# Kernel optimization log

Measured on AMD Instinct MI355X. Metric: run time of the kernel, lower is better.

The kernel has to match this reference:

```python
import jax, jax.numpy as jnp
import numpy as np

D_MODEL = 2048
N_HEADS = 16
QK_ROPE = 64
QK_NOPE = 128
KV_LORA = 512
V_DIM = 128
QK_DIM = QK_ROPE + QK_NOPE
RMS_EPS = 1.1920928955078125e-07  # torch fp32 finfo.eps (nn.RMSNorm default eps=None)


def apply_rope(x, base=10000.0):
    # x: [B, S, H, D] ; torchtune-style interleaved-pair rotary
    B, S, H, D = x.shape
    freqs = 1.0 / (base ** (jnp.arange(0, D, 2, dtype=jnp.float32) / D))  # [D/2]
    t = jnp.arange(S, dtype=jnp.float32)[:, None] * freqs[None, :]        # [S, D/2]
    cos = jnp.cos(t)[None, :, None, :]
    sin = jnp.sin(t)[None, :, None, :]
    x1 = x[..., 0::2]
    x2 = x[..., 1::2]
    out = jnp.stack([x1 * cos - x2 * sin, x2 * cos + x1 * sin], axis=-1)
    return out.reshape(B, S, H, D).astype(x.dtype)


def setup_inputs() -> dict:
    key = jax.random.key(0)
    ks = jax.random.split(key, 6)
    s = lambda fan_in: 1.0 / np.sqrt(fan_in)
    x = jax.random.normal(ks[0], (2, 2048, D_MODEL), dtype=jnp.float32)
    Wq = jax.random.normal(ks[1], (D_MODEL, N_HEADS * QK_DIM), dtype=jnp.float32) * s(D_MODEL)
    Wkv_a = jax.random.normal(ks[2], (D_MODEL, KV_LORA + QK_ROPE), dtype=jnp.float32) * s(D_MODEL)
    kv_norm_w = jnp.ones((KV_LORA,), dtype=jnp.float32)
    Wkv_b = jax.random.normal(ks[3], (KV_LORA, N_HEADS * (QK_NOPE + V_DIM)), dtype=jnp.float32) * s(KV_LORA)
    Wo = jax.random.normal(ks[4], (N_HEADS * V_DIM, D_MODEL), dtype=jnp.float32) * s(N_HEADS * V_DIM)
    return {"x": x, "Wq": Wq, "Wkv_a": Wkv_a, "kv_norm_w": kv_norm_w, "Wkv_b": Wkv_b, "Wo": Wo}


def reference(x, Wq, Wkv_a, kv_norm_w, Wkv_b, Wo):
    B, S, _ = x.shape
    # queries: split nope/rope, rotary on rope slice only
    q = (x @ Wq).reshape(B, S, N_HEADS, QK_DIM)
    q_nope, q_rope = q[..., :QK_NOPE], q[..., QK_NOPE:]
    q = jnp.concatenate([q_nope, apply_rope(q_rope)], axis=-1)  # [B,S,H,QK_DIM]
    # compressed kv + decoupled rope key
    kv = x @ Wkv_a                                              # [B,S,KV_LORA+QK_ROPE]
    c_kv, k_rope = kv[..., :KV_LORA], kv[..., KV_LORA:]
    k_rope = apply_rope(k_rope.reshape(B, S, 1, QK_ROPE))       # [B,S,1,QK_ROPE]
    # RMSNorm on compressed latent, then decompress
    c_kv = c_kv * jax.lax.rsqrt(jnp.mean(c_kv * c_kv, axis=-1, keepdims=True) + RMS_EPS) * kv_norm_w
    kv = (c_kv @ Wkv_b).reshape(B, S, N_HEADS, QK_NOPE + V_DIM)
    k_nope, v = kv[..., :QK_NOPE], kv[..., QK_NOPE:]
    k = jnp.concatenate([k_nope, jnp.broadcast_to(k_rope, (B, S, N_HEADS, QK_ROPE))], axis=-1)
    # causal SDPA over sequence dim
    scale = 1.0 / np.sqrt(QK_DIM)
    scores = jnp.einsum('bqhd,bkhd->bhqk', q, k) * scale        # [B,H,S,S]
    mask = jnp.tril(jnp.ones((S, S), dtype=bool))
    scores = jnp.where(mask, scores, jnp.finfo(scores.dtype).min)
    attn = jax.nn.softmax(scores, axis=-1)
    out = jnp.einsum('bhqk,bkhd->bqhd', attn, v).reshape(B, S, N_HEADS * V_DIM)
    return out @ Wo
```

## Files before the change

kernel.cpp:

```cpp
#include <hip/hip_runtime.h>
#include <hip/hip_bf16.h>
#include <math.h>

#define BATCH   2
#define SEQ     2048
#define DM      2048
#define NH      16
#define QKR     64
#define QKN     128
#define KVL     512
#define VD      128
#define QKD     192
#define KVA_LD  640
#define RMS_EPS 1.1920928955078125e-07f

typedef __bf16 bf16x8 __attribute__((ext_vector_type(8)));
typedef float  f32x4  __attribute__((ext_vector_type(4)));

__device__ __forceinline__ void async16(const __bf16* g, __bf16* l)
{
    __builtin_amdgcn_global_load_lds(
        (__attribute__((address_space(1))) unsigned int*)g,
        (__attribute__((address_space(3))) unsigned int*)l,
        16, 0, 0);
}

__global__ __launch_bounds__(256) void f32_to_bf16(const float* __restrict__ src,
                                                   __bf16* __restrict__ dst)
{
    int i = (blockIdx.x * 256 + threadIdx.x) * 4;
    float4 v = *reinterpret_cast<const float4*>(src + i);
    dst[i + 0] = (__bf16)v.x;
    dst[i + 1] = (__bf16)v.y;
    dst[i + 2] = (__bf16)v.z;
    dst[i + 3] = (__bf16)v.w;
}

__global__ __launch_bounds__(256) void transpose_w(const float* __restrict__ W,
                                                   __bf16* __restrict__ Wt,
                                                   int K, int N)
{
    __shared__ float t[64][65];
    const int n0 = blockIdx.x * 64, k0 = blockIdx.y * 64;
    const int tid = threadIdx.x;
    #pragma unroll
    for (int i = 0; i < 16; ++i) {
        int flat = i * 256 + tid;
        int kl = flat >> 6, nl = flat & 63;
        t[kl][nl] = (n0 + nl < N) ? W[(size_t)(k0 + kl) * N + n0 + nl] : 0.f;
    }
    __syncthreads();
    #pragma unroll
    for (int i = 0; i < 16; ++i) {
        int flat = i * 256 + tid;
        int nl = flat >> 6, kl = flat & 63;
        Wt[(size_t)(n0 + nl) * K + k0 + kl] = (__bf16)t[kl][nl];
    }
}

template<typename OT>
__global__ __launch_bounds__(256) void gemm_bf16(const __bf16* __restrict__ A,
                                                 const __bf16* __restrict__ Bt,
                                                 OT* __restrict__ C,
                                                 int K, int lda, int ldb, int ldc)
{
    __shared__ __bf16 As[128 * 32];
    __shared__ __bf16 Bs[128 * 32];
    const int tid = threadIdx.x;
    const int lane = tid & 63, wave = tid >> 6;
    const int n = lane & 15, quad = lane >> 4;
    const int row0 = blockIdx.y * 128, col0 = blockIdx.x * 128;
    const int wm = (wave >> 1) * 64, wn = (wave & 1) * 64;

    f32x4 acc[4][4];
    #pragma unroll
    for (int mi = 0; mi < 4; ++mi)
        #pragma unroll
        for (int ni = 0; ni < 4; ++ni)
            #pragma unroll
            for (int r = 0; r < 4; ++r) acc[mi][ni][r] = 0.f;

    const __bf16* Ag0 = A  + (size_t)(row0 + (tid >> 2)) * lda + (tid & 3) * 8;
    const __bf16* Bg0 = Bt + (size_t)(col0 + (tid >> 2)) * ldb + (tid & 3) * 8;
    const __bf16* Ag1 = Ag0 + (size_t)64 * lda;
    const __bf16* Bg1 = Bg0 + (size_t)64 * ldb;
    __bf16* As0 = As + tid * 8;        __bf16* As1 = As + (tid + 256) * 8;
    __bf16* Bs0 = Bs + tid * 8;        __bf16* Bs1 = Bs + (tid + 256) * 8;

    for (int k0 = 0; k0 < K; k0 += 32) {
        __syncthreads();
        async16(Ag0 + k0, As0);
        async16(Ag1 + k0, As1);
        async16(Bg0 + k0, Bs0);
        async16(Bg1 + k0, Bs1);
        __syncthreads();

        bf16x8 af[4], bfr[4];
        #pragma unroll
        for (int mi = 0; mi < 4; ++mi)
            af[mi] = *reinterpret_cast<const bf16x8*>(&As[(wm + mi * 16 + n) * 32 + quad * 8]);
        #pragma unroll
        for (int ni = 0; ni < 4; ++ni)
            bfr[ni] = *reinterpret_cast<const bf16x8*>(&Bs[(wn + ni * 16 + n) * 32 + quad * 8]);
        #pragma unroll
        for (int mi = 0; mi < 4; ++mi)
            #pragma unroll
            for (int ni = 0; ni < 4; ++ni)
                acc[mi][ni] = __builtin_amdgcn_mfma_f32_16x16x32_bf16(af[mi], bfr[ni], acc[mi][ni], 0, 0, 0);
    }

    #pragma unroll
    for (int mi = 0; mi < 4; ++mi)
        #pragma unroll
        for (int r = 0; r < 4; ++r) {
            OT* cp = C + (size_t)(row0 + wm + mi * 16 + quad * 4 + r) * ldc + col0 + wn + n;
            #pragma unroll
            for (int ni = 0; ni < 4; ++ni)
                cp[ni * 16] = (OT)acc[mi][ni][r];
        }
}

__global__ __launch_bounds__(256) void rope_q_kernel(__bf16* __restrict__ q)
{
    int idx = blockIdx.x * 256 + threadIdx.x;
    int i = idx & 31;
    int h = (idx >> 5) & 15;
    int s = (idx >> 9) & 2047;
    int b = idx >> 20;
    float t = (float)s * __expf(-(float)(2 * i) / 64.0f * 9.210340371976184f);
    float c = __cosf(t), sn = __sinf(t);
    __bf16* p = q + ((size_t)(b * SEQ + s)) * (NH * QKD) + h * QKD + QKN + 2 * i;
    float x1 = (float)p[0], x2 = (float)p[1];
    p[0] = (__bf16)(x1 * c - x2 * sn);
    p[1] = (__bf16)(x2 * c + x1 * sn);
}

__global__ __launch_bounds__(256) void rope_k_kernel(const float* __restrict__ kva,
                                                     __bf16* __restrict__ krope)
{
    int idx = blockIdx.x * 256 + threadIdx.x;
    int i = idx & 31;
    int s = (idx >> 5) & 2047;
    int b = idx >> 16;
    float t = (float)s * __expf(-(float)(2 * i) / 64.0f * 9.210340371976184f);
    float c = __cosf(t), sn = __sinf(t);
    const float* p = kva + ((size_t)(b * SEQ + s)) * KVA_LD + KVL + 2 * i;
    float x1 = p[0], x2 = p[1];
    __bf16* o = krope + ((size_t)(b * SEQ + s)) * QKR + 2 * i;
    o[0] = (__bf16)(x1 * c - x2 * sn);
    o[1] = (__bf16)(x2 * c + x1 * sn);
}

__global__ __launch_bounds__(256) void rmsnorm_kernel(const float* __restrict__ kva,
                                                      const float* __restrict__ w,
                                                      __bf16* __restrict__ out)
{
    const int rid = blockIdx.x;
    const float* row = kva + (size_t)rid * KVA_LD;
    const int tid = threadIdx.x;
    float v[2];
    float ss = 0.f;
    #pragma unroll
    for (int j = 0; j < 2; ++j) {
        int d = tid + j * 256;
        v[j] = row[d];
        ss += v[j] * v[j];
    }
    #pragma unroll
    for (int off = 32; off > 0; off >>= 1) ss += __shfl_down(ss, off, 64);
    __shared__ float red[4];
    if ((tid & 63) == 0) red[tid >> 6] = ss;
    __syncthreads();
    float total = red[0] + red[1] + red[2] + red[3];
    float scale = 1.0f / sqrtf(total * (1.0f / KVL) + RMS_EPS);
    #pragma unroll
    for (int j = 0; j < 2; ++j) {
        int d = tid + j * 256;
        out[(size_t)rid * KVL + d] = (__bf16)(v[j] * scale * w[d]);
    }
}

__global__ __launch_bounds__(256) void build_vt(const __bf16* __restrict__ kvb,
                                                __bf16* __restrict__ Vt)
{
    __shared__ __bf16 tile[64][136];
    const int s0 = blockIdx.x * 64, h = blockIdx.y, b = blockIdx.z;
    const int t = threadIdx.x;
    #pragma unroll
    for (int i = 0; i < 4; ++i) {
        int flat = i * 256 + t;
        int sl = flat >> 4, c8 = flat & 15;
        bf16x8 v = *reinterpret_cast<const bf16x8*>(
            &kvb[((size_t)(b * SEQ + s0 + sl)) * (NH * 256) + h * 256 + 128 + c8 * 8]);
        *reinterpret_cast<bf16x8*>(&tile[sl][c8 * 8]) = v;
    }
    __syncthreads();
    #pragma unroll
    for (int j = 0; j < 32; ++j) {
        int flat = j * 256 + t;
        int d = flat >> 6, sl = flat & 63;
        Vt[((size_t)((b * NH + h) * VD + d)) * SEQ + s0 + sl] = tile[sl][d];
    }
}

#define LKS 216
#define LVS 72
#define LPS 72
__global__ __launch_bounds__(256, 2) void attn_mfma(const __bf16* __restrict__ qb,
                                                    const __bf16* __restrict__ kvb,
                                                    const __bf16* __restrict__ krope,
                                                    const __bf16* __restrict__ Vt,
                                                    __bf16* __restrict__ ob)
{
    __shared__ __bf16 Ks[64 * LKS];
    __shared__ __bf16 Vs[128 * LVS];
    __shared__ __bf16 Ps[2][4 * 16 * LPS];
    const int tid = threadIdx.x;
    const int wave = tid >> 6, lane = tid & 63;
    const int n = lane & 15, quad = lane >> 4;
    const int pair = blockIdx.x, h = blockIdx.y, b = blockIdx.z;
    const int bh = b * NH + h;
    const float scale = 0.07216878364870323f;
    int qs[2];
    qs[0] = pair; qs[1] = 31 - pair;
    const int ntmax = qs[1] + 1;

    bf16x8 qfrag[2][6];
    #pragma unroll
    for (int s = 0; s < 2; ++s) {
        const int qrow = qs[s] * 64 + wave * 16 + n;
        const __bf16* qp = qb + ((size_t)(b * SEQ + qrow)) * (NH * QKD) + h * QKD + quad * 8;
        #pragma unroll
        for (int c = 0; c < 6; ++c)
            qfrag[s][c] = *reinterpret_cast<const bf16x8*>(qp + c * 32);
    }

    f32x4 Oa[2][8];
    float m_i[2][4], l_i[2][4];
    #pragma unroll
    for (int s = 0; s < 2; ++s) {
        #pragma unroll
        for (int i = 0; i < 8; ++i)
            #pragma unroll
            for (int r = 0; r < 4; ++r) Oa[s][i][r] = 0.f;
        #pragma unroll
        for (int r = 0; r < 4; ++r) { m_i[s][r] = -1e30f; l_i[s][r] = 0.f; }
    }

    int kkey[6], kc8[6];
    #pragma unroll
    for (int i = 0; i < 6; ++i) {
        int flat = i * 256 + tid;
        kkey[i] = flat / 24; kc8[i] = flat % 24;
    }
    const int vd = tid >> 3, vc8 = tid & 7;

    const __bf16* Vg = Vt + (size_t)bh * VD * SEQ;

    bf16x8 kpre[6], vpre[4];
    {
        const int k0 = 0;
        #pragma unroll
        for (int i = 0; i < 6; ++i) {
            const __bf16* src = (kc8[i] < 16)
                ? kvb + ((size_t)(b * SEQ + k0 + kkey[i])) * (NH * 256) + h * 256 + kc8[i] * 8
                : krope + ((size_t)(b * SEQ + k0 + kkey[i])) * QKR + (kc8[i] - 16) * 8;
            kpre[i] = *reinterpret_cast<const bf16x8*>(src);
        }
        #pragma unroll
        for (int i = 0; i < 4; ++i)
            vpre[i] = *reinterpret_cast<const bf16x8*>(Vg + (size_t)(vd + i * 32) * SEQ + k0 + vc8 * 8);
    }

    for (int kt = 0; kt < ntmax; ++kt) {
        __syncthreads();
        #pragma unroll
        for (int i = 0; i < 6; ++i)
            *reinterpret_cast<bf16x8*>(&Ks[kkey[i] * LKS + kc8[i] * 8]) = kpre[i];
        #pragma unroll
        for (int i = 0; i < 4; ++i)
            *reinterpret_cast<bf16x8*>(&Vs[(vd + i * 32) * LVS + vc8 * 8]) = vpre[i];
        __syncthreads();

        if (kt + 1 < ntmax) {
            const int k0n = (kt + 1) * 64;
            #pragma unroll
            for (int i = 0; i < 6; ++i) {
                const __bf16* src = (kc8[i] < 16)
                    ? kvb + ((size_t)(b * SEQ + k0n + kkey[i])) * (NH * 256) + h * 256 + kc8[i] * 8
                    : krope + ((size_t)(b * SEQ + k0n + kkey[i])) * QKR + (kc8[i] - 16) * 8;
                kpre[i] = *reinterpret_cast<const bf16x8*>(src);
            }
            #pragma unroll
            for (int i = 0; i < 4; ++i)
                vpre[i] = *reinterpret_cast<const bf16x8*>(Vg + (size_t)(vd + i * 32) * SEQ + k0n + vc8 * 8);
        }

        const int k0 = kt * 64;
        #pragma unroll
        for (int s = 0; s < 2; ++s) {
            if (kt > qs[s]) continue;

            f32x4 sacc[4];
            #pragma unroll
            for (int t = 0; t < 4; ++t) {
                f32x4 a;
                #pragma unroll
                for (int r = 0; r < 4; ++r) a[r] = 0.f;
                #pragma unroll
                for (int c = 0; c < 6; ++c) {
                    bf16x8 kf = *reinterpret_cast<const bf16x8*>(&Ks[(t * 16 + n) * LKS + c * 32 + quad * 8]);
                    a = __builtin_amdgcn_mfma_f32_16x16x32_bf16(qfrag[s][c], kf, a, 0, 0, 0);
                }
                sacc[t] = a;
            }

            const int qg = qs[s] * 64 + wave * 16 + quad * 4;
            const bool diag = (kt == qs[s]);
            float mloc[4];
            #pragma unroll
            for (int r = 0; r < 4; ++r) mloc[r] = -1e30f;
            #pragma unroll
            for (int t = 0; t < 4; ++t) {
                int key = k0 + t * 16 + n;
                #pragma unroll
                for (int r = 0; r < 4; ++r) {
                    float sv = sacc[t][r] * scale;
                    if (diag) sv = (key <= qg + r) ? sv : -1e30f;
                    sacc[t][r] = sv;
                    mloc[r] = fmaxf(mloc[r], sv);
                }
            }
            #pragma unroll
            for (int off = 1; off < 16; off <<= 1)
                #pragma unroll
                for (int r = 0; r < 4; ++r)
                    mloc[r] = fmaxf(mloc[r], __shfl_xor(mloc[r], off, 64));
            float alpha[4], sum[4];
            #pragma unroll
            for (int r = 0; r < 4; ++r) {
                float mn = fmaxf(m_i[s][r], mloc[r]);
                alpha[r] = __expf(m_i[s][r] - mn);
                m_i[s][r] = mn;
                sum[r] = 0.f;
            }
            #pragma unroll
            for (int t = 0; t < 4; ++t)
                #pragma unroll
                for (int r = 0; r < 4; ++r) {
                    float p = __expf(sacc[t][r] - m_i[s][r]);
                    sum[r] += p;
                    Ps[s][wave * 16 * LPS + (quad * 4 + r) * LPS + t * 16 + n] = (__bf16)p;
                }
            #pragma unroll
            for (int off = 1; off < 16; off <<= 1)
                #pragma unroll
                for (int r = 0; r < 4; ++r)
                    sum[r] += __shfl_xor(sum[r], off, 64);
            #pragma unroll
            for (int r = 0; r < 4; ++r) l_i[s][r] = l_i[s][r] * alpha[r] + sum[r];
            #pragma unroll
            for (int i = 0; i < 8; ++i)
                #pragma unroll
                for (int r = 0; r < 4; ++r) Oa[s][i][r] *= alpha[r];

            __asm__ volatile("s_waitcnt lgkmcnt(0)" ::: "memory");

            #pragma unroll
            for (int kc = 0; kc < 2; ++kc) {
                bf16x8 pf = *reinterpret_cast<const bf16x8*>(&Ps[s][wave * 16 * LPS + n * LPS + kc * 32 + quad * 8]);
                #pragma unroll
                for (int vt = 0; vt < 8; ++vt) {
                    bf16x8 vf = *reinterpret_cast<const bf16x8*>(&Vs[(vt * 16 + n) * LVS + kc * 32 + quad * 8]);
                    Oa[s][vt] = __builtin_amdgcn_mfma_f32_16x16x32_bf16(pf, vf, Oa[s][vt], 0, 0, 0);
                }
            }
        }
    }

    #pragma unroll
    for (int s = 0; s < 2; ++s)
        #pragma unroll
        for (int r = 0; r < 4; ++r) {
            float inv = 1.0f / l_i[s][r];
            int row = qs[s] * 64 + wave * 16 + quad * 4 + r;
            __bf16* op = ob + ((size_t)(b * SEQ + row)) * (NH * VD) + h * VD;
            #pragma unroll
            for (int vt = 0; vt < 8; ++vt)
                op[vt * 16 + n] = (__bf16)(Oa[s][vt][r] * inv);
        }
}

extern "C" void kernel_launch(void* const* d_in, const int* in_sizes, int n_in,
                              void* d_out, int out_size, void* d_ws, size_t ws_size,
                              hipStream_t stream)
{
    const float* x         = (const float*)d_in[0];
    const float* Wq        = (const float*)d_in[1];
    const float* Wkv_a     = (const float*)d_in[2];
    const float* kv_norm_w = (const float*)d_in[3];
    const float* Wkv_b     = (const float*)d_in[4];
    const float* Wo        = (const float*)d_in[5];
    float* out = (float*)d_out;

    float* ws = (float*)d_ws;
    __bf16* q_bf   = (__bf16*)ws;
    float*  kv_a   = ws + 6291456;
    __bf16* kv_b   = (__bf16*)(ws + 8912896);
    float*  r3     = ws + 17301504;
    __bf16* xb     = (__bf16*)r3;
    __bf16* Vt     = (__bf16*)r3;
    float*  r4     = ws + 21495808;
    __bf16* Wq_t   = (__bf16*)r4;
    __bf16* Wkva_t = (__bf16*)(r4 + 3145728);
    __bf16* Wkvb_t = (__bf16*)(r4 + 3801088);
    __bf16* attn_o = (__bf16*)r4;
    __bf16* Wo_t   = (__bf16*)(ws + 27787264);
    __bf16* c_kv_n = (__bf16*)(ws + 29884416);
    __bf16* krope  = (__bf16*)(ws + 30932992);

    const int M = BATCH * SEQ;
    dim3 blk(256);

    f32_to_bf16<<<(M * DM) / 1024, blk, 0, stream>>>(x, xb);
    transpose_w<<<dim3(3072 / 64, 2048 / 64), blk, 0, stream>>>(Wq, Wq_t, DM, NH * QKD);
    transpose_w<<<dim3(640 / 64, 2048 / 64), blk, 0, stream>>>(Wkv_a, Wkva_t, DM, KVL + QKR);
    transpose_w<<<dim3(4096 / 64, 512 / 64), blk, 0, stream>>>(Wkv_b, Wkvb_t, KVL, NH * 256);
    transpose_w<<<dim3(2048 / 64, 2048 / 64), blk, 0, stream>>>(Wo, Wo_t, NH * VD, DM);

    gemm_bf16<__bf16><<<dim3(3072 / 128, M / 128), blk, 0, stream>>>(xb, Wq_t, q_bf, DM, DM, DM, NH * QKD);
    gemm_bf16<float><<<dim3(640 / 128, M / 128), blk, 0, stream>>>(xb, Wkva_t, kv_a, DM, DM, DM, KVA_LD);

    rope_q_kernel<<<(BATCH * SEQ * NH * 32) / 256, blk, 0, stream>>>(q_bf);
    rope_k_kernel<<<(BATCH * SEQ * 32) / 256, blk, 0, stream>>>(kv_a, krope);
    rmsnorm_kernel<<<M, blk, 0, stream>>>(kv_a, kv_norm_w, c_kv_n);

    gemm_bf16<__bf16><<<dim3(4096 / 128, M / 128), blk, 0, stream>>>(c_kv_n, Wkvb_t, kv_b, KVL, KVL, KVL, NH * 256);

    build_vt<<<dim3(SEQ / 64, NH, BATCH), blk, 0, stream>>>(kv_b, Vt);

    attn_mfma<<<dim3(16, NH, BATCH), blk, 0, stream>>>(q_bf, kv_b, krope, Vt, attn_o);

    gemm_bf16<float><<<dim3(2048 / 128, M / 128), blk, 0, stream>>>(attn_o, Wo_t, out, NH * VD, NH * VD, NH * VD, DM);
}
```

Before: 535.9 us.

## Split paired query strips into one strip per block with higher occupancy

The attention kernel no longer pairs a short and a long causal query strip in one block. Each block now handles a single 64-row strip, launched longest-first, which doubles the grid and halves per-thread register state. This allows three blocks per CU via launch bounds and a smaller K padding. It also raises wave priority around the MFMA sections. Each K/V tile is now loaded once per strip instead of shared across two strips, which adds global traffic, and the block tail is less balanced.

```diff
diff --git a/kernel.cpp b/kernel.cpp
--- a/kernel.cpp
+++ b/kernel.cpp
@@ -203,10 +203,10 @@
     }
 }
 
-#define LKS 216
+#define LKS 200
 #define LVS 72
 #define LPS 72
-__global__ __launch_bounds__(256, 2) void attn_mfma(const __bf16* __restrict__ qb,
+__global__ __launch_bounds__(256, 3) void attn_mfma(const __bf16* __restrict__ qb,
                                                     const __bf16* __restrict__ kvb,
                                                     const __bf16* __restrict__ krope,
                                                     const __bf16* __restrict__ Vt,
@@ -214,38 +214,33 @@
 {
     __shared__ __bf16 Ks[64 * LKS];
     __shared__ __bf16 Vs[128 * LVS];
-    __shared__ __bf16 Ps[2][4 * 16 * LPS];
+    __shared__ __bf16 Ps[4 * 16 * LPS];
     const int tid = threadIdx.x;
     const int wave = tid >> 6, lane = tid & 63;
     const int n = lane & 15, quad = lane >> 4;
-    const int pair = blockIdx.x, h = blockIdx.y, b = blockIdx.z;
+    const int strip = 31 - blockIdx.x;
+    const int h = blockIdx.y, b = blockIdx.z;
     const int bh = b * NH + h;
     const float scale = 0.07216878364870323f;
-    int qs[2];
-    qs[0] = pair; qs[1] = 31 - pair;
-    const int ntmax = qs[1] + 1;
-
-    bf16x8 qfrag[2][6];
-    #pragma unroll
-    for (int s = 0; s < 2; ++s) {
-        const int qrow = qs[s] * 64 + wave * 16 + n;
+    const int nt = strip + 1;
+
+    bf16x8 qfrag[6];
+    {
+        const int qrow = strip * 64 + wave * 16 + n;
         const __bf16* qp = qb + ((size_t)(b * SEQ + qrow)) * (NH * QKD) + h * QKD + quad * 8;
         #pragma unroll
         for (int c = 0; c < 6; ++c)
-            qfrag[s][c] = *reinterpret_cast<const bf16x8*>(qp + c * 32);
-    }
-
-    f32x4 Oa[2][8];
-    float m_i[2][4], l_i[2][4];
-    #pragma unroll
-    for (int s = 0; s < 2; ++s) {
-        #pragma unroll
-        for (int i = 0; i < 8; ++i)
-            #pragma unroll
-            for (int r = 0; r < 4; ++r) Oa[s][i][r] = 0.f;
-        #pragma unroll
-        for (int r = 0; r < 4; ++r) { m_i[s][r] = -1e30f; l_i[s][r] = 0.f; }
-    }
+            qfrag[c] = *reinterpret_cast<const bf16x8*>(qp + c * 32);
+    }
+
+    f32x4 Oa[8];
+    float m_i[4], l_i[4];
+    #pragma unroll
+    for (int i = 0; i < 8; ++i)
+        #pragma unroll
+        for (int r = 0; r < 4; ++r) Oa[i][r] = 0.f;
+    #pragma unroll
+    for (int r = 0; r < 4; ++r) { m_i[r] = -1e30f; l_i[r] = 0.f; }
 
     int kkey[6], kc8[6];
     #pragma unroll
@@ -272,7 +267,7 @@
             vpre[i] = *reinterpret_cast<const bf16x8*>(Vg + (size_t)(vd + i * 32) * SEQ + k0 + vc8 * 8);
     }
 
-    for (int kt = 0; kt < ntmax; ++kt) {
+    for (int kt = 0; kt < nt; ++kt) {
         __syncthreads();
         #pragma unroll
         for (int i = 0; i < 6; ++i)
@@ -282,7 +277,7 @@
             *reinterpret_cast<bf16x8*>(&Vs[(vd + i * 32) * LVS + vc8 * 8]) = vpre[i];
         __syncthreads();
 
-        if (kt + 1 < ntmax) {
+        if (kt + 1 < nt) {
             const int k0n = (kt + 1) * 64;
             #pragma unroll
             for (int i = 0; i < 6; ++i) {
@@ -297,98 +292,96 @@
         }
 
         const int k0 = kt * 64;
-        #pragma unroll
-        for (int s = 0; s < 2; ++s) {
-            if (kt > qs[s]) continue;
-
-            f32x4 sacc[4];
-            #pragma unroll
-            for (int t = 0; t < 4; ++t) {
-                f32x4 a;
-                #pragma unroll
-                for (int r = 0; r < 4; ++r) a[r] = 0.f;
-                #pragma unroll
-                for (int c = 0; c < 6; ++c) {
-                    bf16x8 kf = *reinterpret_cast<const bf16x8*>(&Ks[(t * 16 + n) * LKS + c * 32 + quad * 8]);
-                    a = __builtin_amdgcn_mfma_f32_16x16x32_bf16(qfrag[s][c], kf, a, 0, 0, 0);
-                }
-                sacc[t] = a;
+
+        f32x4 sacc[4];
+        __builtin_amdgcn_s_setprio(1);
+        #pragma unroll
+        for (int t = 0; t < 4; ++t) {
+            f32x4 a;
+            #pragma unroll
+            for (int r = 0; r < 4; ++r) a[r] = 0.f;
+            #pragma unroll
+            for (int c = 0; c < 6; ++c) {
+                bf16x8 kf = *reinterpret_cast<const bf16x8*>(&Ks[(t * 16 + n) * LKS + c * 32 + quad * 8]);
+                a = __builtin_amdgcn_mfma_f32_16x16x32_bf16(qfrag[c], kf, a, 0, 0, 0);
             }
-
-            const int qg = qs[s] * 64 + wave * 16 + quad * 4;
-            const bool diag = (kt == qs[s]);
-            float mloc[4];
-            #pragma unroll
-            for (int r = 0; r < 4; ++r) mloc[r] = -1e30f;
-            #pragma unroll
-            for (int t = 0; t < 4; ++t) {
-                int key = k0 + t * 16 + n;
-                #pragma unroll
-                for (int r = 0; r < 4; ++r) {
-                    float sv = sacc[t][r] * scale;
-                    if (diag) sv = (key <= qg + r) ? sv : -1e30f;
-                    sacc[t][r] = sv;
-                    mloc[r] = fmaxf(mloc[r], sv);
-                }
+            sacc[t] = a;
+        }
+        __builtin_amdgcn_s_setprio(0);
+
+        const int qg = strip * 64 + wave * 16 + quad * 4;
+        const bool diag = (kt == strip);
+        float mloc[4];
+        #pragma unroll
+        for (int r = 0; r < 4; ++r) mloc[r] = -1e30f;
+        #pragma unroll
+        for (int t = 0; t < 4; ++t) {
+            int key = k0 + t * 16 + n;
+            #pragma unroll
+            for (int r = 0; r < 4; ++r) {
+                float sv = sacc[t][r] * scale;
+                if (diag) sv = (key <= qg + r) ? sv : -1e30f;
+                sacc[t][r] = sv;
+                mloc[r] = fmaxf(mloc[r], sv);
             }
-            #pragma unroll
-            for (int off = 1; off < 16; off <<= 1)
-                #pragma unroll
-                for (int r = 0; r < 4; ++r)
-                    mloc[r] = fmaxf(mloc[r], __shfl_xor(mloc[r], off, 64));
-            float alpha[4], sum[4];
+        }
+        #pragma unroll
+        for (int off = 1; off < 16; off <<= 1)
+            #pragma unroll
+            for (int r = 0; r < 4; ++r)
+                mloc[r] = fmaxf(mloc[r], __shfl_xor(mloc[r], off, 64));
+        float alpha[4], sum[4];
+        #pragma unroll
+        for (int r = 0; r < 4; ++r) {
+            float mn = fmaxf(m_i[r], mloc[r]);
+            alpha[r] = __expf(m_i[r] - mn);
+            m_i[r] = mn;
+            sum[r] = 0.f;
+        }
+        #pragma unroll
+        for (int t = 0; t < 4; ++t)
             #pragma unroll
             for (int r = 0; r < 4; ++r) {
-                float mn = fmaxf(m_i[s][r], mloc[r]);
-                alpha[r] = __expf(m_i[s][r] - mn);
-                m_i[s][r] = mn;
-                sum[r] = 0.f;
+                float p = __expf(sacc[t][r] - m_i[r]);
+                sum[r] += p;
+                Ps[wave * 16 * LPS + (quad * 4 + r) * LPS + t * 16 + n] = (__bf16)p;
             }
-            #pragma unroll
-            for (int t = 0; t < 4; ++t)
-                #pragma unroll
-                for (int r = 0; r < 4; ++r) {
-                    float p = __expf(sacc[t][r] - m_i[s][r]);
-                    sum[r] += p;
-                    Ps[s][wave * 16 * LPS + (quad * 4 + r) * LPS + t * 16 + n] = (__bf16)p;
-                }
-            #pragma unroll
-            for (int off = 1; off < 16; off <<= 1)
-                #pragma unroll
-                for (int r = 0; r < 4; ++r)
-                    sum[r] += __shfl_xor(sum[r], off, 64);
-            #pragma unroll
-            for (int r = 0; r < 4; ++r) l_i[s][r] = l_i[s][r] * alpha[r] + sum[r];
-            #pragma unroll
-            for (int i = 0; i < 8; ++i)
-                #pragma unroll
-                for (int r = 0; r < 4; ++r) Oa[s][i][r] *= alpha[r];
-
-            __asm__ volatile("s_waitcnt lgkmcnt(0)" ::: "memory");
-
-            #pragma unroll
-            for (int kc = 0; kc < 2; ++kc) {
-                bf16x8 pf = *reinterpret_cast<const bf16x8*>(&Ps[s][wave * 16 * LPS + n * LPS + kc * 32 + quad * 8]);
-                #pragma unroll
-                for (int vt = 0; vt < 8; ++vt) {
-                    bf16x8 vf = *reinterpret_cast<const bf16x8*>(&Vs[(vt * 16 + n) * LVS + kc * 32 + quad * 8]);
-                    Oa[s][vt] = __builtin_amdgcn_mfma_f32_16x16x32_bf16(pf, vf, Oa[s][vt], 0, 0, 0);
-                }
+        #pragma unroll
+        for (int off = 1; off < 16; off <<= 1)
+            #pragma unroll
+            for (int r = 0; r < 4; ++r)
+                sum[r] += __shfl_xor(sum[r], off, 64);
+        #pragma unroll
+        for (int r = 0; r < 4; ++r) l_i[r] = l_i[r] * alpha[r] + sum[r];
+        #pragma unroll
+        for (int i = 0; i < 8; ++i)
+            #pragma unroll
+            for (int r = 0; r < 4; ++r) Oa[i][r] *= alpha[r];
+
+        __asm__ volatile("s_waitcnt lgkmcnt(0)" ::: "memory");
+
+        __builtin_amdgcn_s_setprio(1);
+        #pragma unroll
+        for (int kc = 0; kc < 2; ++kc) {
+            bf16x8 pf = *reinterpret_cast<const bf16x8*>(&Ps[wave * 16 * LPS + n * LPS + kc * 32 + quad * 8]);
+            #pragma unroll
+            for (int vt = 0; vt < 8; ++vt) {
+                bf16x8 vf = *reinterpret_cast<const bf16x8*>(&Vs[(vt * 16 + n) * LVS + kc * 32 + quad * 8]);
+                Oa[vt] = __builtin_amdgcn_mfma_f32_16x16x32_bf16(pf, vf, Oa[vt], 0, 0, 0);
             }
         }
-    }
-
-    #pragma unroll
-    for (int s = 0; s < 2; ++s)
-        #pragma unroll
-        for (int r = 0; r < 4; ++r) {
-            float inv = 1.0f / l_i[s][r];
-            int row = qs[s] * 64 + wave * 16 + quad * 4 + r;
-            __bf16* op = ob + ((size_t)(b * SEQ + row)) * (NH * VD) + h * VD;
-            #pragma unroll
-            for (int vt = 0; vt < 8; ++vt)
-                op[vt * 16 + n] = (__bf16)(Oa[s][vt][r] * inv);
-        }
+        __builtin_amdgcn_s_setprio(0);
+    }
+
+    #pragma unroll
+    for (int r = 0; r < 4; ++r) {
+        float inv = 1.0f / l_i[r];
+        int row = strip * 64 + wave * 16 + quad * 4 + r;
+        __bf16* op = ob + ((size_t)(b * SEQ + row)) * (NH * VD) + h * VD;
+        #pragma unroll
+        for (int vt = 0; vt < 8; ++vt)
+            op[vt * 16 + n] = (__bf16)(Oa[vt][r] * inv);
+    }
 }
 
 extern "C" void kernel_launch(void* const* d_in, const int* in_sizes, int n_in,
@@ -439,7 +432,7 @@
 
     build_vt<<<dim3(SEQ / 64, NH, BATCH), blk, 0, stream>>>(kv_b, Vt);
 
-    attn_mfma<<<dim3(16, NH, BATCH), blk, 0, stream>>>(q_bf, kv_b, krope, Vt, attn_o);
+    attn_mfma<<<dim3(32, NH, BATCH), blk, 0, stream>>>(q_bf, kv_b, krope, Vt, attn_o);
 
     gemm_bf16<float><<<dim3(2048 / 128, M / 128), blk, 0, stream>>>(attn_o, Wo_t, out, NH * VD, NH * VD, NH * VD, DM);
 }
```

Measured after the change: 641.0 us. +19.6%, slower.

## Double GEMM K-tile to 64 and XOR-swizzle LDS layout

Applied to the files above, without the earlier changes.

The bf16 GEMM now stages 64-wide K slices per iteration instead of 32, halving the number of barrier pairs per K loop. LDS rows are XOR-swizzled in 16-byte chunks on both the async global-to-LDS store and the fragment reads, to cut LDS bank conflicts. LDS use per block doubles to 32 KB, which may lower occupancy, and the kernel still has no double buffering, so loads and MFMAs do not overlap.

```diff
diff --git a/kernel.cpp b/kernel.cpp
--- a/kernel.cpp
+++ b/kernel.cpp
@@ -64,8 +64,8 @@
                                                  OT* __restrict__ C,
                                                  int K, int lda, int ldb, int ldc)
 {
-    __shared__ __bf16 As[128 * 32];
-    __shared__ __bf16 Bs[128 * 32];
+    __shared__ __bf16 As[128 * 64];
+    __shared__ __bf16 Bs[128 * 64];
     const int tid = threadIdx.x;
     const int lane = tid & 63, wave = tid >> 6;
     const int n = lane & 15, quad = lane >> 4;
@@ -80,33 +80,49 @@
             #pragma unroll
             for (int r = 0; r < 4; ++r) acc[mi][ni][r] = 0.f;
 
-    const __bf16* Ag0 = A  + (size_t)(row0 + (tid >> 2)) * lda + (tid & 3) * 8;
-    const __bf16* Bg0 = Bt + (size_t)(col0 + (tid >> 2)) * ldb + (tid & 3) * 8;
-    const __bf16* Ag1 = Ag0 + (size_t)64 * lda;
-    const __bf16* Bg1 = Bg0 + (size_t)64 * ldb;
-    __bf16* As0 = As + tid * 8;        __bf16* As1 = As + (tid + 256) * 8;
-    __bf16* Bs0 = Bs + tid * 8;        __bf16* Bs1 = Bs + (tid + 256) * 8;
-
-    for (int k0 = 0; k0 < K; k0 += 32) {
+    const int srow = tid >> 3;
+    const int scol8p = tid & 7;
+    const __bf16* Ag[4]; const __bf16* Bg[4];
+    #pragma unroll
+    for (int i = 0; i < 4; ++i) {
+        int row = srow + i * 32;
+        int col8l = scol8p ^ (row & 7);
+        Ag[i] = A  + (size_t)(row0 + row) * lda + col8l * 8;
+        Bg[i] = Bt + (size_t)(col0 + row) * ldb + col8l * 8;
+    }
+    __bf16* Asd = As + tid * 8;
+    __bf16* Bsd = Bs + tid * 8;
+
+    for (int k0 = 0; k0 < K; k0 += 64) {
         __syncthreads();
-        async16(Ag0 + k0, As0);
-        async16(Ag1 + k0, As1);
-        async16(Bg0 + k0, Bs0);
-        async16(Bg1 + k0, Bs1);
+        #pragma unroll
+        for (int i = 0; i < 4; ++i) {
+            async16(Ag[i] + k0, Asd + i * 2048);
+            async16(Bg[i] + k0, Bsd + i * 2048);
+        }
         __syncthreads();
 
-        bf16x8 af[4], bfr[4];
-        #pragma unroll
-        for (int mi = 0; mi < 4; ++mi)
-            af[mi] = *reinterpret_cast<const bf16x8*>(&As[(wm + mi * 16 + n) * 32 + quad * 8]);
-        #pragma unroll
-        for (int ni = 0; ni < 4; ++ni)
-            bfr[ni] = *reinterpret_cast<const bf16x8*>(&Bs[(wn + ni * 16 + n) * 32 + quad * 8]);
-        #pragma unroll
-        for (int mi = 0; mi < 4; ++mi)
-            #pragma unroll
-            for (int ni = 0; ni < 4; ++ni)
-                acc[mi][ni] = __builtin_amdgcn_mfma_f32_16x16x32_bf16(af[mi], bfr[ni], acc[mi][ni], 0, 0, 0);
+        #pragma unroll
+        for (int kc = 0; kc < 2; ++kc) {
+            bf16x8 af[4], bfr[4];
+            #pragma unroll
+            for (int mi = 0; mi < 4; ++mi) {
+                int row = wm + mi * 16 + n;
+                int slot = (kc * 4 + quad) ^ (row & 7);
+                af[mi] = *reinterpret_cast<const bf16x8*>(&As[row * 64 + slot * 8]);
+            }
+            #pragma unroll
+            for (int ni = 0; ni < 4; ++ni) {
+                int row = wn + ni * 16 + n;
+                int slot = (kc * 4 + quad) ^ (row & 7);
+                bfr[ni] = *reinterpret_cast<const bf16x8*>(&Bs[row * 64 + slot * 8]);
+            }
+            #pragma unroll
+            for (int mi = 0; mi < 4; ++mi)
+                #pragma unroll
+                for (int ni = 0; ni < 4; ++ni)
+                    acc[mi][ni] = __builtin_amdgcn_mfma_f32_16x16x32_bf16(af[mi], bfr[ni], acc[mi][ni], 0, 0, 0);
+        }
     }
 
     #pragma unroll
```

After: 506.9 us. 1.06x faster.
